# Optimization experiments

Measured on AMD Instinct MI355X. Metric: run time of the kernel, lower is better.

The kernel has to match this reference:

```python
import jax, jax.numpy as jnp
import numpy as np

NEG_SLOPE = 0.2  # LeakyReLU slope used by GAT attention
EPS = 1e-16


def gat_conv(x, edge_index, W, a_src, a_dst, b):
    """One GATConv layer with 'mean' head aggregation.
    x: [N, Fin], edge_index: [2, E] (row 0 = src/j, row 1 = dst/i),
    W: [Fin, H*F], a_src/a_dst: [H, F], b: [F].
    Returns [N, F].
    """
    N = x.shape[0]
    H, F = a_src.shape
    h = (x @ W).reshape(N, H, F)                      # [N, H, F]
    src, dst = edge_index[0], edge_index[1]
    # per-node attention halves, gathered per edge
    as_ = jnp.einsum('nhf,hf->nh', h, a_src)          # [N, H]
    ad_ = jnp.einsum('nhf,hf->nh', h, a_dst)          # [N, H]
    e = jax.nn.leaky_relu(as_[src] + ad_[dst], NEG_SLOPE)  # [E, H]
    # segment softmax over incoming edges of each dst node
    m = jax.ops.segment_max(e, dst, num_segments=N)   # [N, H]
    ex = jnp.exp(e - m[dst])                          # [E, H]
    denom = jax.ops.segment_sum(ex, dst, num_segments=N)
    alpha = ex / (denom[dst] + EPS)                   # [E, H]
    # weighted scatter-aggregate of source features
    out = jax.ops.segment_sum(alpha[:, :, None] * h[src], dst, num_segments=N)  # [N, H, F]
    return out.mean(axis=1) + b                       # mean over heads


def setup_inputs() -> dict:
    key = jax.random.key(0)
    ks = jax.random.split(key, 10)
    N, E = 100000, 1000000
    in_dim, hid, out_dim, H = 128, 32, 16, 4
    x = jax.random.normal(ks[0], (N, in_dim), dtype=jnp.float32)
    edge_index = jax.random.randint(ks[1], (2, E), 0, N, dtype=jnp.int64)
    s1 = 1.0 / np.sqrt(in_dim)
    s2 = 1.0 / np.sqrt(hid)
    W1 = jax.random.uniform(ks[2], (in_dim, H * hid), jnp.float32, -s1, s1)
    a1_src = jax.random.uniform(ks[3], (H, hid), jnp.float32, -s2, s2)
    a1_dst = jax.random.uniform(ks[4], (H, hid), jnp.float32, -s2, s2)
    b1 = jnp.zeros((hid,), jnp.float32)
    s3 = 1.0 / np.sqrt(out_dim)
    W2 = jax.random.uniform(ks[5], (hid, H * out_dim), jnp.float32, -s2, s2)
    a2_src = jax.random.uniform(ks[6], (H, out_dim), jnp.float32, -s3, s3)
    a2_dst = jax.random.uniform(ks[7], (H, out_dim), jnp.float32, -s3, s3)
    b2 = jnp.zeros((out_dim,), jnp.float32)
    return {"x": x, "edge_index": edge_index,
            "W1": W1, "a1_src": a1_src, "a1_dst": a1_dst, "b1": b1,
            "W2": W2, "a2_src": a2_src, "a2_dst": a2_dst, "b2": b2}


def reference(x, edge_index, W1, a1_src, a1_dst, b1, W2, a2_src, a2_dst, b2):
    h = gat_conv(x, edge_index, W1, a1_src, a1_dst, b1)
    h = jax.nn.relu(h)
    # dropout is identity in eval mode
    out = gat_conv(h, edge_index, W2, a2_src, a2_dst, b2)
    return out
```

## Files before the change

kernel.cpp:

```cpp
#include <hip/hip_runtime.h>
#include <math.h>

#define NEG_SLOPE 0.2f
#define EPS_GAT 1e-16f
#define LOG2E 1.4426950408889634f
typedef unsigned int u32;
typedef unsigned short u16;
typedef __attribute__((ext_vector_type(8))) short short8;
typedef __attribute__((ext_vector_type(4))) float f32x4;

__device__ inline u16 f2bf(float x) {
    union { float f; u32 u; } v; v.f = x;
    u32 r = v.u + 0x7FFFu + ((v.u >> 16) & 1u);
    return (u16)(r >> 16);
}
__device__ inline float bf_lo(u32 u) {
    union { u32 i; float f; } v; v.i = u << 16; return v.f;
}
__device__ inline float bf_hi(u32 u) {
    union { u32 i; float f; } v; v.i = u & 0xFFFF0000u; return v.f;
}
__device__ inline float bf1(u16 s) {
    union { u32 i; float f; } v; v.i = ((u32)s) << 16; return v.f;
}
__device__ inline float fast_exp2(float x) {
#if __has_builtin(__builtin_amdgcn_exp2f)
    return __builtin_amdgcn_exp2f(x);
#else
    return exp2f(x);
#endif
}
__device__ inline float lrelu_exp2(float t) {
    return fast_exp2(fmaxf(t, NEG_SLOPE * t));
}


__global__ void degree_prep_kernel(const int* __restrict__ dst, int E,
                                   int* __restrict__ counts, int* __restrict__ rank,
                                   const float* __restrict__ W1,
                                   u16* __restrict__ w1t_hi, u16* __restrict__ w1t_lo,
                                   const float* __restrict__ W2, const float* __restrict__ a2s,
                                   const float* __restrict__ a2d, float* __restrict__ w_as,
                                   float* __restrict__ w_ad, int degBlocks) {
    int b = blockIdx.x;
    if (b < degBlocks) {
        int e = b * 256 + threadIdx.x;
        if (e < E) rank[e] = atomicAdd(&counts[dst[e]], 1);
    } else if (b < degBlocks + 64) {
        int i = (b - degBlocks) * 256 + threadIdx.x;
        int k = i >> 7, n = i & 127;
        float w = W1[i];
        u16 hi = f2bf(w);
        u16 lo = f2bf(w - bf1(hi));
        w1t_hi[n * 128 + k] = hi;
        w1t_lo[n * 128 + k] = lo;
    } else {
        int t = threadIdx.x;
        if (t < 128) {
            int h = t >> 5, k = t & 31;
            float s1 = 0.f, s2 = 0.f;
#pragma unroll
            for (int f = 0; f < 16; ++f) {
                float w = W2[k * 64 + h * 16 + f];
                s1 += w * a2s[h * 16 + f];
                s2 += w * a2d[h * 16 + f];
            }
            w_as[h * 32 + k] = s1;
            w_ad[h * 32 + k] = s2;
        }
    }
}

__global__ __launch_bounds__(1024) void scan_block_kernel(const int* __restrict__ counts, int N,
                                                          int* __restrict__ scanned, int* __restrict__ bsums) {
    __shared__ int tmp[1024];
    int i = blockIdx.x * 1024 + threadIdx.x;
    int v = (i < N) ? counts[i] : 0;
    tmp[threadIdx.x] = v;
    __syncthreads();
    for (int d = 1; d < 1024; d <<= 1) {
        int t = (threadIdx.x >= d) ? tmp[threadIdx.x - d] : 0;
        __syncthreads();
        tmp[threadIdx.x] += t;
        __syncthreads();
    }
    if (i < N) scanned[i] = tmp[threadIdx.x];
    if (threadIdx.x == 1023) bsums[blockIdx.x] = tmp[1023];
}

__global__ __launch_bounds__(256) void scan_partials_kernel(int* __restrict__ bsums, int nb) {
    __shared__ int tmp[256];
    int tid = threadIdx.x;
    int v = (tid < nb) ? bsums[tid] : 0;
    tmp[tid] = v;
    __syncthreads();
    for (int d = 1; d < 256; d <<= 1) {
        int t = (tid >= d) ? tmp[tid - d] : 0;
        __syncthreads();
        tmp[tid] += t;
        __syncthreads();
    }
    if (tid < nb) bsums[tid] = tmp[tid] - v;
}

__global__ void finalize_offsets_kernel(const int* __restrict__ scanned,
                                        const int* __restrict__ bsums_excl, int N,
                                        int* __restrict__ row_off) {
    int i = blockIdx.x * blockDim.x + threadIdx.x;
    if (i < N) {
        int incl = scanned[i] + bsums_excl[i >> 10];
        row_off[i + 1] = incl;
        if (i == 0) row_off[0] = 0;
    }
}

__global__ void fill_csr_kernel(const int* __restrict__ src, const int* __restrict__ dst, int E,
                                const int* __restrict__ row_off, const int* __restrict__ rank,
                                int* __restrict__ csr_src) {
    int e = blockIdx.x * blockDim.x + threadIdx.x;
    if (e < E) {
        int pos = row_off[dst[e]] + rank[e];
        csr_src[pos] = src[e];
    }
}


__global__ __launch_bounds__(256) void gemm1_mfma_kernel(const float* __restrict__ X,
                                                         const u16* __restrict__ w1t_hi,
                                                         const u16* __restrict__ w1t_lo,
                                                         const float* __restrict__ a_src,
                                                         const float* __restrict__ a_dst,
                                                         u16* __restrict__ Hb,
                                                         float* __restrict__ as_,
                                                         float* __restrict__ ad_, int N) {
    __shared__ u16 xsh_hi[64][40];
    __shared__ u16 xsh_lo[64][40];
    __shared__ u16 wbuf[10240];
    __shared__ float ash[128], adsh[128];
    u16* wsh_hi = wbuf;
    u16* wsh_lo = wbuf + 5120;
    int tid = threadIdx.x;
    int wave = tid >> 6, lane = tid & 63, quad = lane >> 4;
    int m0 = blockIdx.x * 64;

    if (tid < 128) { ash[tid] = a_src[tid]; adsh[tid] = a_dst[tid]; }

    f32x4 acc[4][2];
#pragma unroll
    for (int rt = 0; rt < 4; ++rt)
#pragma unroll
        for (int ct = 0; ct < 2; ++ct) acc[rt][ct] = (f32x4)(0.f);

    int xrow = tid >> 2, xkq = (tid & 3) * 8;

    for (int k0 = 0; k0 < 128; k0 += 32) {
        {
            int gr = m0 + xrow;
            float f[8];
            *(float4*)&f[0] = (gr < N) ? *(const float4*)(X + (size_t)gr * 128 + k0 + xkq)
                                       : make_float4(0.f, 0.f, 0.f, 0.f);
            *(float4*)&f[4] = (gr < N) ? *(const float4*)(X + (size_t)gr * 128 + k0 + xkq + 4)
                                       : make_float4(0.f, 0.f, 0.f, 0.f);
            u16 hi[8], lo[8];
#pragma unroll
            for (int i = 0; i < 8; ++i) {
                hi[i] = f2bf(f[i]);
                lo[i] = f2bf(f[i] - bf1(hi[i]));
            }
            *(uint4*)&xsh_hi[xrow][xkq] = *(uint4*)hi;
            *(uint4*)&xsh_lo[xrow][xkq] = *(uint4*)lo;
        }
        {
#pragma unroll
            for (int i = 0; i < 2; ++i) {
                int id = tid * 2 + i;
                int n = id >> 2, part = id & 3;
                *(uint4*)&wsh_hi[n * 40 + part * 8] =
                    ((const uint4*)(w1t_hi + n * 128 + k0))[part];
                *(uint4*)&wsh_lo[n * 40 + part * 8] =
                    ((const uint4*)(w1t_lo + n * 128 + k0))[part];
            }
        }
        __syncthreads();

        short8 bhi[2], blo[2];
#pragma unroll
        for (int ct = 0; ct < 2; ++ct) {
            int n = wave * 32 + ct * 16 + (lane & 15);
            bhi[ct] = *(const short8*)&wsh_hi[n * 40 + quad * 8];
            blo[ct] = *(const short8*)&wsh_lo[n * 40 + quad * 8];
        }
#pragma unroll
        for (int rt = 0; rt < 4; ++rt) {
            int m = rt * 16 + (lane & 15);
            short8 ahi = *(const short8*)&xsh_hi[m][quad * 8];
            short8 alo = *(const short8*)&xsh_lo[m][quad * 8];
#pragma unroll
            for (int ct = 0; ct < 2; ++ct) {
                acc[rt][ct] = __builtin_amdgcn_mfma_f32_16x16x32_bf16(ahi, bhi[ct], acc[rt][ct], 0, 0, 0);
                acc[rt][ct] = __builtin_amdgcn_mfma_f32_16x16x32_bf16(alo, bhi[ct], acc[rt][ct], 0, 0, 0);
                acc[rt][ct] = __builtin_amdgcn_mfma_f32_16x16x32_bf16(ahi, blo[ct], acc[rt][ct], 0, 0, 0);
            }
        }
        __syncthreads();
    }

    const int HS = 130;
#pragma unroll
    for (int rt = 0; rt < 4; ++rt)
#pragma unroll
        for (int ct = 0; ct < 2; ++ct) {
            int col = wave * 32 + ct * 16 + (lane & 15);
#pragma unroll
            for (int r = 0; r < 4; ++r) {
                int row = rt * 16 + quad * 4 + r;
                u16 hv = f2bf(acc[rt][ct][r]);
                int gr = m0 + row;
                if (gr < N) Hb[(size_t)gr * 128 + col] = hv;
                wbuf[row * HS + col] = hv;
            }
        }
    __syncthreads();

    {
        int row = tid >> 2, h = tid & 3;
        int gr = m0 + row;
        if (gr < N) {
            const u32* hr = (const u32*)&wbuf[row * HS + h * 32];
            float s1 = 0.f, s2 = 0.f;
#pragma unroll
            for (int q = 0; q < 16; ++q) {
                u32 u = hr[q];
                float flo = bf_lo(u), fhi = bf_hi(u);
                s1 += flo * ash[h * 32 + 2 * q] + fhi * ash[h * 32 + 2 * q + 1];
                s2 += flo * adsh[h * 32 + 2 * q] + fhi * adsh[h * 32 + 2 * q + 1];
            }
            as_[(size_t)gr * 4 + h] = s1 * LOG2E;
            ad_[(size_t)gr * 4 + h] = s2 * LOG2E;
        }
    }
}


__global__ __launch_bounds__(256) void node_agg128_kernel(const u32* __restrict__ Hb,
                                                          const float* __restrict__ as_,
                                                          const float* __restrict__ ad_,
                                                          const int* __restrict__ row_off,
                                                          const int* __restrict__ csr_src,
                                                          const float* __restrict__ bias,
                                                          const float* __restrict__ w_as,
                                                          const float* __restrict__ w_ad,
                                                          u32* __restrict__ O1,
                                                          float* __restrict__ as2,
                                                          float* __restrict__ ad2, int N) {
    int lane = threadIdx.x & 63;
    int node = __builtin_amdgcn_readfirstlane(blockIdx.x * 4 + (threadIdx.x >> 6));
    if (node >= N) return;
    int start = __builtin_amdgcn_readfirstlane(row_off[node]);
    int end   = __builtin_amdgcn_readfirstlane(row_off[node + 1]);
    int deg = end - start;
    int h = lane >> 4;
    float adh = ad_[node * 4 + h];

    int clamp = (deg > 0) ? deg - 1 : 0;
    int vidx = csr_src[start + min(lane, clamp)];
    int m = min(deg, 64);

    float2 acc = make_float2(0.f, 0.f);
    float den = 0.f;
    int j = 0;
    for (; j + 4 <= m; j += 4) {
        int s0 = __builtin_amdgcn_readlane(vidx, j);
        int s1 = __builtin_amdgcn_readlane(vidx, j + 1);
        int s2 = __builtin_amdgcn_readlane(vidx, j + 2);
        int s3 = __builtin_amdgcn_readlane(vidx, j + 3);
        float a0 = as_[s0 * 4 + h], a1 = as_[s1 * 4 + h];
        float a2 = as_[s2 * 4 + h], a3 = as_[s3 * 4 + h];
        u32 u0 = Hb[s0 * 64 + lane];
        u32 u1 = Hb[s1 * 64 + lane];
        u32 u2 = Hb[s2 * 64 + lane];
        u32 u3 = Hb[s3 * 64 + lane];
        float e0 = lrelu_exp2(a0 + adh), e1 = lrelu_exp2(a1 + adh);
        float e2 = lrelu_exp2(a2 + adh), e3 = lrelu_exp2(a3 + adh);
        acc.x = fmaf(e0, bf_lo(u0), acc.x); acc.y = fmaf(e0, bf_hi(u0), acc.y); den += e0;
        acc.x = fmaf(e1, bf_lo(u1), acc.x); acc.y = fmaf(e1, bf_hi(u1), acc.y); den += e1;
        acc.x = fmaf(e2, bf_lo(u2), acc.x); acc.y = fmaf(e2, bf_hi(u2), acc.y); den += e2;
        acc.x = fmaf(e3, bf_lo(u3), acc.x); acc.y = fmaf(e3, bf_hi(u3), acc.y); den += e3;
    }
    for (; j < m; ++j) {
        int s = __builtin_amdgcn_readlane(vidx, j);
        float e = lrelu_exp2(as_[s * 4 + h] + adh);
        u32 u = Hb[s * 64 + lane];
        acc.x = fmaf(e, bf_lo(u), acc.x); acc.y = fmaf(e, bf_hi(u), acc.y); den += e;
    }
    for (int jj = start + 64; jj < end; ++jj) {
        int s = __builtin_amdgcn_readfirstlane(csr_src[jj]);
        float e = lrelu_exp2(as_[s * 4 + h] + adh);
        u32 u = Hb[s * 64 + lane];
        acc.x = fmaf(e, bf_lo(u), acc.x); acc.y = fmaf(e, bf_hi(u), acc.y); den += e;
    }
    float inv = 1.f / (den + EPS_GAT);
    float px = acc.x * inv, py = acc.y * inv;
    px += __shfl_xor(px, 16); py += __shfl_xor(py, 16);
    px += __shfl_xor(px, 32); py += __shfl_xor(py, 32);

    int f2 = (lane & 15) * 2;
    float2 bv = *(const float2*)&bias[f2];
    float ox = fmaxf(px * 0.25f + bv.x, 0.f);
    float oy = fmaxf(py * 0.25f + bv.y, 0.f);
    if (lane < 16)
        O1[node * 16 + lane] = (u32)f2bf(ox) | ((u32)f2bf(oy) << 16);

    int h2 = lane >> 4;
    float2 wa = *(const float2*)&w_as[h2 * 32 + f2];
    float2 wd = *(const float2*)&w_ad[h2 * 32 + f2];
    float ta = ox * wa.x + oy * wa.y;
    float td = ox * wd.x + oy * wd.y;
    ta += __shfl_xor(ta, 1); td += __shfl_xor(td, 1);
    ta += __shfl_xor(ta, 2); td += __shfl_xor(td, 2);
    ta += __shfl_xor(ta, 4); td += __shfl_xor(td, 4);
    ta += __shfl_xor(ta, 8); td += __shfl_xor(td, 8);
    if ((lane & 15) == 0) {
        as2[node * 4 + h2] = ta * LOG2E;
        ad2[node * 4 + h2] = td * LOG2E;
    }
}


__global__ __launch_bounds__(256) void node_agg32_fused_kernel(const u32* __restrict__ O1,
                                                               const float* __restrict__ as_,
                                                               const float* __restrict__ ad_,
                                                               const int* __restrict__ row_off,
                                                               const int* __restrict__ csr_src,
                                                               const float* __restrict__ W2,
                                                               const float* __restrict__ b2,
                                                               float* __restrict__ Out, int N) {
    __shared__ float w2sh[2048];
    __shared__ float aggsh[4][136];
    int tid = threadIdx.x;
    {
        float4 v = ((const float4*)W2)[tid];
        *(float4*)&w2sh[tid * 4] = v;
        float4 v2 = ((const float4*)W2)[tid + 256];
        *(float4*)&w2sh[(tid + 256) * 4] = v2;
    }

    int lane = tid & 63;
    int nb = tid >> 6;
    int node = __builtin_amdgcn_readfirstlane(blockIdx.x * 4 + nb);
    bool active = node < N;
    int h = lane >> 4, f = lane & 15;
    if (active) {
        int start = __builtin_amdgcn_readfirstlane(row_off[node]);
        int end   = __builtin_amdgcn_readfirstlane(row_off[node + 1]);
        int deg = end - start;
        float adh = ad_[node * 4 + h];

        int clamp = (deg > 0) ? deg - 1 : 0;
        int vidx = csr_src[start + min(lane, clamp)];
        int m = min(deg, 64);

        float2 acc = make_float2(0.f, 0.f);
        float den = 0.f;
        int j = 0;
        for (; j + 4 <= m; j += 4) {
            int s0 = __builtin_amdgcn_readlane(vidx, j);
            int s1 = __builtin_amdgcn_readlane(vidx, j + 1);
            int s2 = __builtin_amdgcn_readlane(vidx, j + 2);
            int s3 = __builtin_amdgcn_readlane(vidx, j + 3);
            float a0 = as_[s0 * 4 + h], a1 = as_[s1 * 4 + h];
            float a2 = as_[s2 * 4 + h], a3 = as_[s3 * 4 + h];
            u32 u0 = O1[s0 * 16 + f];
            u32 u1 = O1[s1 * 16 + f];
            u32 u2 = O1[s2 * 16 + f];
            u32 u3 = O1[s3 * 16 + f];
            float e0 = lrelu_exp2(a0 + adh), e1 = lrelu_exp2(a1 + adh);
            float e2 = lrelu_exp2(a2 + adh), e3 = lrelu_exp2(a3 + adh);
            acc.x = fmaf(e0, bf_lo(u0), acc.x); acc.y = fmaf(e0, bf_hi(u0), acc.y); den += e0;
            acc.x = fmaf(e1, bf_lo(u1), acc.x); acc.y = fmaf(e1, bf_hi(u1), acc.y); den += e1;
            acc.x = fmaf(e2, bf_lo(u2), acc.x); acc.y = fmaf(e2, bf_hi(u2), acc.y); den += e2;
            acc.x = fmaf(e3, bf_lo(u3), acc.x); acc.y = fmaf(e3, bf_hi(u3), acc.y); den += e3;
        }
        for (; j < m; ++j) {
            int s = __builtin_amdgcn_readlane(vidx, j);
            float e = lrelu_exp2(as_[s * 4 + h] + adh);
            u32 u = O1[s * 16 + f];
            acc.x = fmaf(e, bf_lo(u), acc.x); acc.y = fmaf(e, bf_hi(u), acc.y); den += e;
        }
        for (int jj = start + 64; jj < end; ++jj) {
            int s = __builtin_amdgcn_readfirstlane(csr_src[jj]);
            float e = lrelu_exp2(as_[s * 4 + h] + adh);
            u32 u = O1[s * 16 + f];
            acc.x = fmaf(e, bf_lo(u), acc.x); acc.y = fmaf(e, bf_hi(u), acc.y); den += e;
        }
        float inv = 1.f / (den + EPS_GAT);
        aggsh[nb][h * 34 + f * 2]     = acc.x * inv;
        aggsh[nb][h * 34 + f * 2 + 1] = acc.y * inv;
    }
    __syncthreads();

    if (active) {
        int q = h, o = f;
        float s = 0.f;
#pragma unroll
        for (int k = 0; k < 32; ++k)
            s += aggsh[nb][q * 34 + k] * w2sh[k * 64 + q * 16 + o];
        s += __shfl_xor(s, 16);
        s += __shfl_xor(s, 32);
        if (lane < 16)
            Out[(size_t)node * 16 + o] = s * 0.25f + b2[o];
    }
}


extern "C" void kernel_launch(void* const* d_in, const int* in_sizes, int n_in,
                              void* d_out, int out_size, void* d_ws, size_t ws_size,
                              hipStream_t stream) {
    const float* x      = (const float*)d_in[0];
    const int*   eidx   = (const int*)d_in[1];
    const float* W1     = (const float*)d_in[2];
    const float* a1_src = (const float*)d_in[3];
    const float* a1_dst = (const float*)d_in[4];
    const float* b1     = (const float*)d_in[5];
    const float* W2     = (const float*)d_in[6];
    const float* a2_src = (const float*)d_in[7];
    const float* a2_dst = (const float*)d_in[8];
    const float* b2     = (const float*)d_in[9];
    float* out = (float*)d_out;

    const int N = in_sizes[0] / 128;
    const int E = in_sizes[1] / 2;
    const int* src = eidx;
    const int* dst = eidx + E;

    char* base = (char*)d_ws;
    size_t off = 0;
    auto carve = [&](size_t bytes) -> char* {
        off = (off + 255) & ~(size_t)255;
        char* p = base + off;
        off += bytes;
        return p;
    };
    int* counts   = (int*)carve((size_t)N * 4);
    int* scanned  = (int*)carve((size_t)N * 4);
    int* bsums    = (int*)carve(256 * 4);
    int* row_off  = (int*)carve((size_t)(N + 1) * 4);
    int* rank     = (int*)carve((size_t)E * 4);
    int* csr_src  = (int*)carve((size_t)E * 4);
    u16* w1t_hi   = (u16*)carve(128 * 128 * 2);
    u16* w1t_lo   = (u16*)carve(128 * 128 * 2);
    u16* h1b      = (u16*)carve((size_t)N * 128 * 2);
    u32* out1b    = (u32*)carve((size_t)N * 16 * 4);
    float* as1  = (float*)carve((size_t)N * 4 * 4);
    float* ad1  = (float*)carve((size_t)N * 4 * 4);
    float* as2  = (float*)carve((size_t)N * 4 * 4);
    float* ad2  = (float*)carve((size_t)N * 4 * 4);
    float* w_as = (float*)carve(4 * 32 * 4);
    float* w_ad = (float*)carve(4 * 32 * 4);
    (void)ws_size; (void)n_in; (void)out_size;

    hipMemsetAsync(counts, 0, (size_t)N * 4, stream);
    int degBlocks = (E + 255) / 256;
    degree_prep_kernel<<<degBlocks + 65, 256, 0, stream>>>(dst, E, counts, rank,
                                                           W1, w1t_hi, w1t_lo,
                                                           W2, a2_src, a2_dst, w_as, w_ad,
                                                           degBlocks);
    int nb = (N + 1023) / 1024;
    scan_block_kernel<<<nb, 1024, 0, stream>>>(counts, N, scanned, bsums);
    scan_partials_kernel<<<1, 256, 0, stream>>>(bsums, nb);
    finalize_offsets_kernel<<<(N + 255) / 256, 256, 0, stream>>>(scanned, bsums, N, row_off);
    fill_csr_kernel<<<(E + 255) / 256, 256, 0, stream>>>(src, dst, E, row_off, rank, csr_src);

    gemm1_mfma_kernel<<<(N + 63) / 64, 256, 0, stream>>>(x, w1t_hi, w1t_lo, a1_src, a1_dst,
                                                         h1b, as1, ad1, N);
    node_agg128_kernel<<<(N + 3) / 4, 256, 0, stream>>>((const u32*)h1b, as1, ad1,
                                                        row_off, csr_src, b1, w_as, w_ad,
                                                        out1b, as2, ad2, N);

    node_agg32_fused_kernel<<<(N + 3) / 4, 256, 0, stream>>>(out1b, as2, ad2, row_off,
                                                             csr_src, W2, b2, out, N);
}
```

Baseline: 297.6 us.

## Precompute edge attention weights in parallel across lanes and persist layer-2 aggregation

In both aggregation kernels, attention logits and exponentials for the first 64 incoming edges are computed once in parallel across the 16 lanes of each head group. They are then broadcast with shuffles in the gather loop, which removes the per-edge serialized as_ loads and exp work, and the denominator comes from a shuffle reduction. The layer-2 kernel becomes a grid-stride persistent kernel with W2 columns held in registers and the projection done via shuffles, dropping shared memory and the block barrier. This adds register pressure and shuffle traffic in exchange.

```diff
diff --git a/kernel.cpp b/kernel.cpp
--- a/kernel.cpp
+++ b/kernel.cpp
@@ -260,43 +260,63 @@
     int end   = __builtin_amdgcn_readfirstlane(row_off[node + 1]);
     int deg = end - start;
     int h = lane >> 4;
+    int r = lane & 15;
+    int grpbase = lane & 48;
     float adh = ad_[node * 4 + h];
 
     int clamp = (deg > 0) ? deg - 1 : 0;
-    int vidx = csr_src[start + min(lane, clamp)];
+    int vidx = (deg > 0) ? csr_src[start + min(lane, clamp)] : 0;
     int m = min(deg, 64);
 
+    float Pv[4];
+#pragma unroll
+    for (int q = 0; q < 4; ++q) {
+        int eq = q * 16 + r;
+        int sq = __shfl(vidx, eq);
+        float aq = as_[sq * 4 + h];
+        float pe = lrelu_exp2(aq + adh);
+        Pv[q] = (eq < m) ? pe : 0.f;
+    }
+    float den = (Pv[0] + Pv[1]) + (Pv[2] + Pv[3]);
+    den += __shfl_xor(den, 1);
+    den += __shfl_xor(den, 2);
+    den += __shfl_xor(den, 4);
+    den += __shfl_xor(den, 8);
+
     float2 acc = make_float2(0.f, 0.f);
-    float den = 0.f;
     int j = 0;
-    for (; j + 4 <= m; j += 4) {
-        int s0 = __builtin_amdgcn_readlane(vidx, j);
-        int s1 = __builtin_amdgcn_readlane(vidx, j + 1);
-        int s2 = __builtin_amdgcn_readlane(vidx, j + 2);
-        int s3 = __builtin_amdgcn_readlane(vidx, j + 3);
-        float a0 = as_[s0 * 4 + h], a1 = as_[s1 * 4 + h];
-        float a2 = as_[s2 * 4 + h], a3 = as_[s3 * 4 + h];
-        u32 u0 = Hb[s0 * 64 + lane];
-        u32 u1 = Hb[s1 * 64 + lane];
-        u32 u2 = Hb[s2 * 64 + lane];
-        u32 u3 = Hb[s3 * 64 + lane];
-        float e0 = lrelu_exp2(a0 + adh), e1 = lrelu_exp2(a1 + adh);
-        float e2 = lrelu_exp2(a2 + adh), e3 = lrelu_exp2(a3 + adh);
-        acc.x = fmaf(e0, bf_lo(u0), acc.x); acc.y = fmaf(e0, bf_hi(u0), acc.y); den += e0;
-        acc.x = fmaf(e1, bf_lo(u1), acc.x); acc.y = fmaf(e1, bf_hi(u1), acc.y); den += e1;
-        acc.x = fmaf(e2, bf_lo(u2), acc.x); acc.y = fmaf(e2, bf_hi(u2), acc.y); den += e2;
-        acc.x = fmaf(e3, bf_lo(u3), acc.x); acc.y = fmaf(e3, bf_hi(u3), acc.y); den += e3;
-    }
-    for (; j < m; ++j) {
-        int s = __builtin_amdgcn_readlane(vidx, j);
-        float e = lrelu_exp2(as_[s * 4 + h] + adh);
-        u32 u = Hb[s * 64 + lane];
-        acc.x = fmaf(e, bf_lo(u), acc.x); acc.y = fmaf(e, bf_hi(u), acc.y); den += e;
+#pragma unroll
+    for (int q = 0; q < 4; ++q) {
+        const int lim = min(m, (q + 1) * 16);
+        for (; j + 4 <= lim; j += 4) {
+            int s0 = __builtin_amdgcn_readlane(vidx, j);
+            int s1 = __builtin_amdgcn_readlane(vidx, j + 1);
+            int s2 = __builtin_amdgcn_readlane(vidx, j + 2);
+            int s3 = __builtin_amdgcn_readlane(vidx, j + 3);
+            float e0 = __shfl(Pv[q], grpbase | (j - q * 16));
+            float e1 = __shfl(Pv[q], grpbase | (j + 1 - q * 16));
+            float e2 = __shfl(Pv[q], grpbase | (j + 2 - q * 16));
+            float e3 = __shfl(Pv[q], grpbase | (j + 3 - q * 16));
+            u32 u0 = Hb[(size_t)s0 * 64 + lane];
+            u32 u1 = Hb[(size_t)s1 * 64 + lane];
+            u32 u2 = Hb[(size_t)s2 * 64 + lane];
+            u32 u3 = Hb[(size_t)s3 * 64 + lane];
+            acc.x = fmaf(e0, bf_lo(u0), acc.x); acc.y = fmaf(e0, bf_hi(u0), acc.y);
+            acc.x = fmaf(e1, bf_lo(u1), acc.x); acc.y = fmaf(e1, bf_hi(u1), acc.y);
+            acc.x = fmaf(e2, bf_lo(u2), acc.x); acc.y = fmaf(e2, bf_hi(u2), acc.y);
+            acc.x = fmaf(e3, bf_lo(u3), acc.x); acc.y = fmaf(e3, bf_hi(u3), acc.y);
+        }
+        for (; j < lim; ++j) {
+            int s = __builtin_amdgcn_readlane(vidx, j);
+            float e = __shfl(Pv[q], grpbase | (j - q * 16));
+            u32 u = Hb[(size_t)s * 64 + lane];
+            acc.x = fmaf(e, bf_lo(u), acc.x); acc.y = fmaf(e, bf_hi(u), acc.y);
+        }
     }
     for (int jj = start + 64; jj < end; ++jj) {
         int s = __builtin_amdgcn_readfirstlane(csr_src[jj]);
         float e = lrelu_exp2(as_[s * 4 + h] + adh);
-        u32 u = Hb[s * 64 + lane];
+        u32 u = Hb[(size_t)s * 64 + lane];
         acc.x = fmaf(e, bf_lo(u), acc.x); acc.y = fmaf(e, bf_hi(u), acc.y); den += e;
     }
     float inv = 1.f / (den + EPS_GAT);
@@ -335,80 +355,94 @@
                                                                const float* __restrict__ W2,
                                                                const float* __restrict__ b2,
                                                                float* __restrict__ Out, int N) {
-    __shared__ float w2sh[2048];
-    __shared__ float aggsh[4][136];
-    int tid = threadIdx.x;
-    {
-        float4 v = ((const float4*)W2)[tid];
-        *(float4*)&w2sh[tid * 4] = v;
-        float4 v2 = ((const float4*)W2)[tid + 256];
-        *(float4*)&w2sh[(tid + 256) * 4] = v2;
-    }
-
-    int lane = tid & 63;
-    int nb = tid >> 6;
-    int node = __builtin_amdgcn_readfirstlane(blockIdx.x * 4 + nb);
-    bool active = node < N;
+    int lane = threadIdx.x & 63;
     int h = lane >> 4, f = lane & 15;
-    if (active) {
+    int grpbase = lane & 48;
+    int wid = blockIdx.x * 4 + (threadIdx.x >> 6);
+    int nw = gridDim.x * 4;
+
+    float wcol[32];
+#pragma unroll
+    for (int k = 0; k < 32; ++k) wcol[k] = W2[k * 64 + lane];
+    float bo = b2[f];
+
+    for (int node = wid; node < N; node += nw) {
         int start = __builtin_amdgcn_readfirstlane(row_off[node]);
         int end   = __builtin_amdgcn_readfirstlane(row_off[node + 1]);
         int deg = end - start;
         float adh = ad_[node * 4 + h];
 
         int clamp = (deg > 0) ? deg - 1 : 0;
-        int vidx = csr_src[start + min(lane, clamp)];
+        int vidx = (deg > 0) ? csr_src[start + min(lane, clamp)] : 0;
         int m = min(deg, 64);
 
+        float Pv[4];
+#pragma unroll
+        for (int q = 0; q < 4; ++q) {
+            int eq = q * 16 + f;
+            int sq = __shfl(vidx, eq);
+            float aq = as_[sq * 4 + h];
+            float pe = lrelu_exp2(aq + adh);
+            Pv[q] = (eq < m) ? pe : 0.f;
+        }
+        float den = (Pv[0] + Pv[1]) + (Pv[2] + Pv[3]);
+        den += __shfl_xor(den, 1);
+        den += __shfl_xor(den, 2);
+        den += __shfl_xor(den, 4);
+        den += __shfl_xor(den, 8);
+
         float2 acc = make_float2(0.f, 0.f);
-        float den = 0.f;
         int j = 0;
-        for (; j + 4 <= m; j += 4) {
-            int s0 = __builtin_amdgcn_readlane(vidx, j);
-            int s1 = __builtin_amdgcn_readlane(vidx, j + 1);
-            int s2 = __builtin_amdgcn_readlane(vidx, j + 2);
-            int s3 = __builtin_amdgcn_readlane(vidx, j + 3);
-            float a0 = as_[s0 * 4 + h], a1 = as_[s1 * 4 + h];
-            float a2 = as_[s2 * 4 + h], a3 = as_[s3 * 4 + h];
-            u32 u0 = O1[s0 * 16 + f];
-            u32 u1 = O1[s1 * 16 + f];
-            u32 u2 = O1[s2 * 16 + f];
-            u32 u3 = O1[s3 * 16 + f];
-            float e0 = lrelu_exp2(a0 + adh), e1 = lrelu_exp2(a1 + adh);
-            float e2 = lrelu_exp2(a2 + adh), e3 = lrelu_exp2(a3 + adh);
-            acc.x = fmaf(e0, bf_lo(u0), acc.x); acc.y = fmaf(e0, bf_hi(u0), acc.y); den += e0;
-            acc.x = fmaf(e1, bf_lo(u1), acc.x); acc.y = fmaf(e1, bf_hi(u1), acc.y); den += e1;
-            acc.x = fmaf(e2, bf_lo(u2), acc.x); acc.y = fmaf(e2, bf_hi(u2), acc.y); den += e2;
-            acc.x = fmaf(e3, bf_lo(u3), acc.x); acc.y = fmaf(e3, bf_hi(u3), acc.y); den += e3;
-        }
-        for (; j < m; ++j) {
-            int s = __builtin_amdgcn_readlane(vidx, j);
-            float e = lrelu_exp2(as_[s * 4 + h] + adh);
-            u32 u = O1[s * 16 + f];
-            acc.x = fmaf(e, bf_lo(u), acc.x); acc.y = fmaf(e, bf_hi(u), acc.y); den += e;
+#pragma unroll
+        for (int q = 0; q < 4; ++q) {
+            const int lim = min(m, (q + 1) * 16);
+            for (; j + 4 <= lim; j += 4) {
+                int s0 = __builtin_amdgcn_readlane(vidx, j);
+                int s1 = __builtin_amdgcn_readlane(vidx, j + 1);
+                int s2 = __builtin_amdgcn_readlane(vidx, j + 2);
+                int s3 = __builtin_amdgcn_readlane(vidx, j + 3);
+                float e0 = __shfl(Pv[q], grpbase | (j - q * 16));
+                float e1 = __shfl(Pv[q], grpbase | (j + 1 - q * 16));
+                float e2 = __shfl(Pv[q], grpbase | (j + 2 - q * 16));
+                float e3 = __shfl(Pv[q], grpbase | (j + 3 - q * 16));
+                u32 u0 = O1[s0 * 16 + f];
+                u32 u1 = O1[s1 * 16 + f];
+                u32 u2 = O1[s2 * 16 + f];
+                u32 u3 = O1[s3 * 16 + f];
+                acc.x = fmaf(e0, bf_lo(u0), acc.x); acc.y = fmaf(e0, bf_hi(u0), acc.y);
+                acc.x = fmaf(e1, bf_lo(u1), acc.x); acc.y = fmaf(e1, bf_hi(u1), acc.y);
+                acc.x = fmaf(e2, bf_lo(u2), acc.x); acc.y = fmaf(e2, bf_hi(u2), acc.y);
+                acc.x = fmaf(e3, bf_lo(u3), acc.x); acc.y = fmaf(e3, bf_hi(u3), acc.y);
+            }
+            for (; j < lim; ++j) {
+                int s = __builtin_amdgcn_readlane(vidx, j);
+                float e = __shfl(Pv[q], grpbase | (j - q * 16));
+                u32 u = O1[s * 16 + f];
+                acc.x = fmaf(e, bf_lo(u), acc.x); acc.y = fmaf(e, bf_hi(u), acc.y);
+            }
         }
         for (int jj = start + 64; jj < end; ++jj) {
             int s = __builtin_amdgcn_readfirstlane(csr_src[jj]);
             float e = lrelu_exp2(as_[s * 4 + h] + adh);
             u32 u = O1[s * 16 + f];
-            acc.x = fmaf(e, bf_lo(u), acc.x); acc.y = fmaf(e, bf_hi(u), acc.y); den += e;
+            acc.x = fmaf(e, bf_lo(u), acc.x); acc.y = fmaf(e, bf_hi(u), acc.y);
+            den += e;
         }
         float inv = 1.f / (den + EPS_GAT);
-        aggsh[nb][h * 34 + f * 2]     = acc.x * inv;
-        aggsh[nb][h * 34 + f * 2 + 1] = acc.y * inv;
-    }
-    __syncthreads();
-
-    if (active) {
-        int q = h, o = f;
+        float px = acc.x * inv, py = acc.y * inv;
+
         float s = 0.f;
 #pragma unroll
-        for (int k = 0; k < 32; ++k)
-            s += aggsh[nb][q * 34 + k] * w2sh[k * 64 + q * 16 + o];
+        for (int k = 0; k < 16; ++k) {
+            float vx = __shfl(px, grpbase | k);
+            float vy = __shfl(py, grpbase | k);
+            s = fmaf(vx, wcol[2 * k], s);
+            s = fmaf(vy, wcol[2 * k + 1], s);
+        }
         s += __shfl_xor(s, 16);
         s += __shfl_xor(s, 32);
         if (lane < 16)
-            Out[(size_t)node * 16 + o] = s * 0.25f + b2[o];
+            Out[(size_t)node * 16 + f] = s * 0.25f + bo;
     }
 }
 
@@ -477,6 +511,7 @@
                                                         row_off, csr_src, b1, w_as, w_ad,
                                                         out1b, as2, ad2, N);
 
-    node_agg32_fused_kernel<<<(N + 3) / 4, 256, 0, stream>>>(out1b, as2, ad2, row_off,
-                                                             csr_src, W2, b2, out, N);
-}
+    int agg2Blocks = 2048;
+    node_agg32_fused_kernel<<<agg2Blocks, 256, 0, stream>>>(out1b, as2, ad2, row_off,
+                                                            csr_src, W2, b2, out, N);
+}
```

Result: slower. 332.4 us (+11.7%).

## Process four edges per step across lane groups in layer-2 aggregation

Applied to the files above, without the earlier changes.

Changes the layer-2 gather kernel so that each of the four 16-lane groups handles a different edge, rather than a different head. Each lane now computes attention for all four heads from a float4 load of the source scores, and the partial sums are combined with xor-shuffle reductions at the end. The aim is to cut the serial per-edge loop length by four and raise memory-level parallelism. In exchange it adds four times the exp work per lane, twelve accumulators, and a shuffle reduction. The overflow path for degree above 64 still runs serially and wastes three of the four groups.

```diff
diff --git a/kernel.cpp b/kernel.cpp
--- a/kernel.cpp
+++ b/kernel.cpp
@@ -349,58 +349,88 @@
     int nb = tid >> 6;
     int node = __builtin_amdgcn_readfirstlane(blockIdx.x * 4 + nb);
     bool active = node < N;
-    int h = lane >> 4, f = lane & 15;
+    int g = lane >> 4, f = lane & 15;
     if (active) {
         int start = __builtin_amdgcn_readfirstlane(row_off[node]);
         int end   = __builtin_amdgcn_readfirstlane(row_off[node + 1]);
         int deg = end - start;
-        float adh = ad_[node * 4 + h];
-
-        int clamp = (deg > 0) ? deg - 1 : 0;
-        int vidx = csr_src[start + min(lane, clamp)];
+        float4 ad4 = *(const float4*)&ad_[(size_t)node * 4];
+
+        int clampi = (deg > 0) ? deg - 1 : 0;
+        int vidx = (deg > 0) ? csr_src[start + min(lane, clampi)] : 0;
         int m = min(deg, 64);
 
-        float2 acc = make_float2(0.f, 0.f);
-        float den = 0.f;
-        int j = 0;
-        for (; j + 4 <= m; j += 4) {
-            int s0 = __builtin_amdgcn_readlane(vidx, j);
-            int s1 = __builtin_amdgcn_readlane(vidx, j + 1);
-            int s2 = __builtin_amdgcn_readlane(vidx, j + 2);
-            int s3 = __builtin_amdgcn_readlane(vidx, j + 3);
-            float a0 = as_[s0 * 4 + h], a1 = as_[s1 * 4 + h];
-            float a2 = as_[s2 * 4 + h], a3 = as_[s3 * 4 + h];
-            u32 u0 = O1[s0 * 16 + f];
-            u32 u1 = O1[s1 * 16 + f];
-            u32 u2 = O1[s2 * 16 + f];
-            u32 u3 = O1[s3 * 16 + f];
-            float e0 = lrelu_exp2(a0 + adh), e1 = lrelu_exp2(a1 + adh);
-            float e2 = lrelu_exp2(a2 + adh), e3 = lrelu_exp2(a3 + adh);
-            acc.x = fmaf(e0, bf_lo(u0), acc.x); acc.y = fmaf(e0, bf_hi(u0), acc.y); den += e0;
-            acc.x = fmaf(e1, bf_lo(u1), acc.x); acc.y = fmaf(e1, bf_hi(u1), acc.y); den += e1;
-            acc.x = fmaf(e2, bf_lo(u2), acc.x); acc.y = fmaf(e2, bf_hi(u2), acc.y); den += e2;
-            acc.x = fmaf(e3, bf_lo(u3), acc.x); acc.y = fmaf(e3, bf_hi(u3), acc.y); den += e3;
-        }
-        for (; j < m; ++j) {
-            int s = __builtin_amdgcn_readlane(vidx, j);
-            float e = lrelu_exp2(as_[s * 4 + h] + adh);
-            u32 u = O1[s * 16 + f];
-            acc.x = fmaf(e, bf_lo(u), acc.x); acc.y = fmaf(e, bf_hi(u), acc.y); den += e;
+        float ax0 = 0.f, ax1 = 0.f, ax2 = 0.f, ax3 = 0.f;
+        float ay0 = 0.f, ay1 = 0.f, ay2 = 0.f, ay3 = 0.f;
+        float d0 = 0.f, d1 = 0.f, d2 = 0.f, d3 = 0.f;
+
+        for (int j = 0; j < m; j += 4) {
+            int sl = __shfl(vidx, j + g);
+            bool valid = (j + g) < m;
+            float4 a4 = *(const float4*)&as_[(size_t)sl * 4];
+            u32 u = O1[(size_t)sl * 16 + f];
+            float e0 = lrelu_exp2(a4.x + ad4.x);
+            float e1 = lrelu_exp2(a4.y + ad4.y);
+            float e2 = lrelu_exp2(a4.z + ad4.z);
+            float e3 = lrelu_exp2(a4.w + ad4.w);
+            e0 = valid ? e0 : 0.f;
+            e1 = valid ? e1 : 0.f;
+            e2 = valid ? e2 : 0.f;
+            e3 = valid ? e3 : 0.f;
+            float ulo = bf_lo(u), uhi = bf_hi(u);
+            ax0 = fmaf(e0, ulo, ax0); ay0 = fmaf(e0, uhi, ay0); d0 += e0;
+            ax1 = fmaf(e1, ulo, ax1); ay1 = fmaf(e1, uhi, ay1); d1 += e1;
+            ax2 = fmaf(e2, ulo, ax2); ay2 = fmaf(e2, uhi, ay2); d2 += e2;
+            ax3 = fmaf(e3, ulo, ax3); ay3 = fmaf(e3, uhi, ay3); d3 += e3;
         }
         for (int jj = start + 64; jj < end; ++jj) {
             int s = __builtin_amdgcn_readfirstlane(csr_src[jj]);
-            float e = lrelu_exp2(as_[s * 4 + h] + adh);
-            u32 u = O1[s * 16 + f];
-            acc.x = fmaf(e, bf_lo(u), acc.x); acc.y = fmaf(e, bf_hi(u), acc.y); den += e;
-        }
-        float inv = 1.f / (den + EPS_GAT);
-        aggsh[nb][h * 34 + f * 2]     = acc.x * inv;
-        aggsh[nb][h * 34 + f * 2 + 1] = acc.y * inv;
+            float4 a4 = *(const float4*)&as_[(size_t)s * 4];
+            u32 u = O1[(size_t)s * 16 + f];
+            float e0 = lrelu_exp2(a4.x + ad4.x);
+            float e1 = lrelu_exp2(a4.y + ad4.y);
+            float e2 = lrelu_exp2(a4.z + ad4.z);
+            float e3 = lrelu_exp2(a4.w + ad4.w);
+            if (g == 0) {
+                float ulo = bf_lo(u), uhi = bf_hi(u);
+                ax0 = fmaf(e0, ulo, ax0); ay0 = fmaf(e0, uhi, ay0); d0 += e0;
+                ax1 = fmaf(e1, ulo, ax1); ay1 = fmaf(e1, uhi, ay1); d1 += e1;
+                ax2 = fmaf(e2, ulo, ax2); ay2 = fmaf(e2, uhi, ay2); d2 += e2;
+                ax3 = fmaf(e3, ulo, ax3); ay3 = fmaf(e3, uhi, ay3); d3 += e3;
+            }
+        }
+
+        ax0 += __shfl_xor(ax0, 16); ax0 += __shfl_xor(ax0, 32);
+        ax1 += __shfl_xor(ax1, 16); ax1 += __shfl_xor(ax1, 32);
+        ax2 += __shfl_xor(ax2, 16); ax2 += __shfl_xor(ax2, 32);
+        ax3 += __shfl_xor(ax3, 16); ax3 += __shfl_xor(ax3, 32);
+        ay0 += __shfl_xor(ay0, 16); ay0 += __shfl_xor(ay0, 32);
+        ay1 += __shfl_xor(ay1, 16); ay1 += __shfl_xor(ay1, 32);
+        ay2 += __shfl_xor(ay2, 16); ay2 += __shfl_xor(ay2, 32);
+        ay3 += __shfl_xor(ay3, 16); ay3 += __shfl_xor(ay3, 32);
+        d0 += __shfl_xor(d0, 16); d0 += __shfl_xor(d0, 32);
+        d1 += __shfl_xor(d1, 16); d1 += __shfl_xor(d1, 32);
+        d2 += __shfl_xor(d2, 16); d2 += __shfl_xor(d2, 32);
+        d3 += __shfl_xor(d3, 16); d3 += __shfl_xor(d3, 32);
+
+        float i0 = 1.f / (d0 + EPS_GAT), i1 = 1.f / (d1 + EPS_GAT);
+        float i2 = 1.f / (d2 + EPS_GAT), i3 = 1.f / (d3 + EPS_GAT);
+        float px0 = ax0 * i0, px1 = ax1 * i1, px2 = ax2 * i2, px3 = ax3 * i3;
+        float py0 = ay0 * i0, py1 = ay1 * i1, py2 = ay2 * i2, py3 = ay3 * i3;
+
+        float wxa = (g & 1) ? px1 : px0;
+        float wxb = (g & 1) ? px3 : px2;
+        float wx  = (g & 2) ? wxb : wxa;
+        float wya = (g & 1) ? py1 : py0;
+        float wyb = (g & 1) ? py3 : py2;
+        float wy  = (g & 2) ? wyb : wya;
+        aggsh[nb][g * 34 + 2 * f]     = wx;
+        aggsh[nb][g * 34 + 2 * f + 1] = wy;
     }
     __syncthreads();
 
     if (active) {
-        int q = h, o = f;
+        int q = g, o = f;
         float s = 0.f;
 #pragma unroll
         for (int k = 0; k < 32; ++k)
```

Result: slower. 308.3 us (+3.6%).
